# Optimization experiments

Hardware: AMD Instinct MI355X
Metric: run time of the kernel (lower is better)

## Reference

```python
import jax, jax.numpy as jnp
import numpy as np

B, M, N, D, H = 4, 8, 128, 32, 64
SMALL_V = 1e-8


def setup_inputs() -> dict:
    key = jax.random.key(0)
    ks = jax.random.split(key, 12)
    s = 0.05
    x = jax.random.normal(ks[0], (B, M, N, D), jnp.float32)
    sizes = jax.random.randint(ks[1], (B,), N // 2, N + 1)
    valid = (jnp.arange(N)[None, :] < sizes[:, None]).astype(jnp.float32)  # [B,N]
    x = x * valid[:, None, :, None]  # zero out padded items
    return {
        "x": x,
        "x_size": sizes.astype(jnp.float32),
        "W1a": jax.random.normal(ks[2], (D, 2 * D), jnp.float32) * s,
        "b1a": jax.random.normal(ks[3], (2 * D,), jnp.float32) * s,
        "W1b": jax.random.normal(ks[4], (2 * D, D), jnp.float32) * s,
        "b1b": jax.random.normal(ks[5], (D,), jnp.float32) * s,
        "W2a": jax.random.normal(ks[6], (D, 2 * D), jnp.float32) * s,
        "b2a": jax.random.normal(ks[7], (2 * D,), jnp.float32) * s,
        "W2b": jax.random.normal(ks[8], (2 * D, H), jnp.float32) * s,
        "b2b": jax.random.normal(ks[9], (H,), jnp.float32) * s,
        "w3": jax.random.normal(ks[10], (H,), jnp.float32) * s,
        "b3": jax.random.normal(ks[11], (1,), jnp.float32) * s,
    }


def _item_mask(x):
    # 1.0 where the item's feature row has any nonzero entry, else 0.0. [...,N,1]
    return jnp.any(x != 0, axis=-1, keepdims=True).astype(x.dtype)


def _set_norm(x, x_size):
    # layer_normalization with is_set_norm=True: normalize over (N*D) per set,
    # dividing by the true valid size x_size*D and masking padded items.
    b, m, n, d = x.shape
    mask = jnp.broadcast_to(_item_mask(x), x.shape).reshape(b, m, n * d)
    xr = x.reshape(b, m, n * d)
    denom = x_size[:, None] * d  # [B,1] -> broadcasts over nSet
    mean = jnp.sum(xr, axis=-1) / denom  # [B,M]
    diff = xr - mean[..., None]
    std = jnp.sqrt(jnp.sum(diff * diff * mask, axis=-1) / denom)  # [B,M]
    out = diff / (std[..., None] + SMALL_V) * mask
    return out.reshape(b, m, n, d)


def reference(x, x_size, W1a, b1a, W1b, b1b, W2a, b2a, W2b, b2b, w3, b3):
    mask = _item_mask(x)  # [B,M,N,1]
    x_orig = x
    xn = _set_norm(x, x_size) * mask  # [B,M,N,D]
    # MLP1 (rank-4 -> masked by its own input's item mask)
    m1 = _item_mask(xn)
    x1 = (jnp.matmul(jax.nn.gelu(jnp.matmul(xn, W1a) + b1a), W1b) + b1b) * m1
    # pairwise differences: x_diff[b,m,i,j,:] = x1[b,m,i,:] - xn[b,m,j,:]
    x_diff = x1[:, :, :, None, :] - xn[:, :, None, :, :]  # [B,M,N,N,D]
    # MLP2 (rank-5 -> no mask, is_SoftMax=0)
    e = jnp.matmul(jax.nn.gelu(jnp.matmul(x_diff, W2a) + b2a), W2b) + b2b  # [B,M,N,N,H]
    # aggregation: out[b,m,j,h,d] = sum_i e[b,m,i,j,h] * x1[b,m,i,d]
    agg = jnp.einsum('bmijh,bmid->bmjhd', e, x1)
    # MLP3_linear: Dense(1) over H, then squeeze
    out = jnp.einsum('bmjhd,h->bmjd', agg, w3) + b3[0]
    out = (out + x_orig) * mask
    return out
```

## Files before the change

### kernel.cpp

```cpp
#include <hip/hip_runtime.h>

#define BMC 32
#define NNC 128
#define DDC 32
#define KKC 64
constexpr int ND = NNC * DDC;
constexpr int NK = NNC * KKC;
constexpr int NS = NNC * NNC;
#define SMALLV 1e-8f

__device__ __forceinline__ float gelu_f(float v) {
    float v2 = v * v;
    float p  = fmaf(0.1029432f, v2, 2.3022082f);
    float e  = __builtin_amdgcn_exp2f(v * p);
    float r  = __builtin_amdgcn_rcpf(e + 1.0f);
    return fmaf(-v, r, v);
}

__global__ __launch_bounds__(256) void mlp_kernel(
    const float* __restrict__ x, const float* __restrict__ x_size,
    const float* __restrict__ W1a, const float* __restrict__ b1a,
    const float* __restrict__ W1b, const float* __restrict__ b1b,
    const float* __restrict__ W2a, const float* __restrict__ b2a,
    const float* __restrict__ W2b, const float* __restrict__ b2b,
    const float* __restrict__ w3,
    float* __restrict__ x1g, float* __restrict__ A1g, float* __restrict__ A2r,
    float* __restrict__ v2g, float* __restrict__ c3g)
{
    __shared__ float sW1a[DDC * KKC];
    __shared__ float sW1b[KKC * DDC];
    __shared__ float sW2a[DDC * KKC];
    __shared__ float sXn[8 * DDC];
    __shared__ float sH[8 * KKC];
    __shared__ float sX1[8 * DDC];
    __shared__ float sB1a[KKC], sB2a[KKC], sB1b[DDC];
    __shared__ float sAny[NNC];
    __shared__ float sRed[4];

    const int t  = threadIdx.x;
    const int bm = blockIdx.x >> 4;
    const int nt = blockIdx.x & 15;
    const int n0 = nt * 8;
    const int w  = t >> 6;

    {
        const float4* a4 = (const float4*)W1a;
        const float4* b4 = (const float4*)W1b;
        const float4* c4 = (const float4*)W2a;
        float4* sa = (float4*)sW1a; float4* sb = (float4*)sW1b; float4* sc = (float4*)sW2a;
        sa[t] = a4[t]; sa[t + 256] = a4[t + 256];
        sb[t] = b4[t]; sb[t + 256] = b4[t + 256];
        sc[t] = c4[t]; sc[t + 256] = c4[t + 256];
    }
    if (t < KKC) { sB1a[t] = b1a[t]; sB2a[t] = b2a[t]; }
    if (t < DDC) { sB1b[t] = b1b[t]; }
    if (t < NNC) sAny[t] = 0.f;
    __syncthreads();

    const float4* xs4 = (const float4*)(x + (size_t)bm * ND);
    float4 v4[4];
    float lsum = 0.f;
    #pragma unroll
    for (int s = 0; s < 4; ++s) {
        int f = t + s * 256;
        float4 q = xs4[f];
        v4[s] = q;
        lsum += q.x + q.y + q.z + q.w;
        if (q.x != 0.f || q.y != 0.f || q.z != 0.f || q.w != 0.f) sAny[f >> 3] = 1.f;
    }
    #pragma unroll
    for (int off = 32; off; off >>= 1) lsum += __shfl_xor(lsum, off);
    if ((t & 63) == 0) sRed[w] = lsum;
    __syncthreads();
    const float xsz   = x_size[bm >> 3];
    const float denom = xsz * (float)DDC;
    const float mean  = (sRed[0] + sRed[1] + sRed[2] + sRed[3]) / denom;

    float lsq = 0.f;
    #pragma unroll
    for (int s = 0; s < 4; ++s) {
        int f = t + s * 256;
        float mk = sAny[f >> 3];
        float dx = v4[s].x - mean, dy = v4[s].y - mean;
        float dz = v4[s].z - mean, dw = v4[s].w - mean;
        lsq += mk * (dx * dx + dy * dy + dz * dz + dw * dw);
    }
    #pragma unroll
    for (int off = 32; off; off >>= 1) lsq += __shfl_xor(lsq, off);
    __syncthreads();
    if ((t & 63) == 0) sRed[w] = lsq;
    __syncthreads();
    const float sq  = sRed[0] + sRed[1] + sRed[2] + sRed[3];
    const float inv = 1.f / (sqrtf(sq / denom) + SMALLV);

    {
        float xv = x[(size_t)bm * ND + n0 * DDC + t];
        sXn[t] = (xv - mean) * inv * sAny[n0 + (t >> 5)];
    }
    __syncthreads();

    const int k = t & 63;

    #pragma unroll
    for (int r = 0; r < 2; ++r) {
        int n = w + r * 4;
        const float* xr = &sXn[n * DDC];
        float acc = sB1a[k];
        #pragma unroll
        for (int d = 0; d < DDC; ++d) acc = fmaf(xr[d], sW1a[d * KKC + k], acc);
        sH[n * KKC + k] = gelu_f(acc);
    }
    __syncthreads();

    {
        const int d2 = t & 31;
        const int n  = t >> 5;
        const float* hr = &sH[n * KKC];
        float acc = sB1b[d2];
        #pragma unroll
        for (int q = 0; q < KKC; ++q) acc = fmaf(hr[q], sW1b[q * DDC + d2], acc);
        float val = acc * sAny[n0 + n];
        sX1[n * DDC + d2] = val;
        x1g[(size_t)bm * ND + (n0 + n) * DDC + d2] = val;
    }
    __syncthreads();

    #pragma unroll
    for (int r = 0; r < 2; ++r) {
        int n = w + r * 4;
        const float* x1r = &sX1[n * DDC];
        const float* xnr = &sXn[n * DDC];
        float a1 = sB2a[k], a2 = 0.f;
        #pragma unroll
        for (int d = 0; d < DDC; ++d) {
            a1 = fmaf(x1r[d], sW2a[d * KKC + k], a1);
            a2 = fmaf(xnr[d], sW2a[d * KKC + k], a2);
        }
        A1g[(size_t)bm * NK + (n0 + n) * KKC + k] = a1;
        A2r[(size_t)bm * NK + (n0 + n) * KKC + k] = a2;
    }

    if (blockIdx.x == 0) {
        int kk = t >> 2, hq = t & 3;
        float p = 0.f;
        #pragma unroll
        for (int h = 0; h < 16; ++h)
            p = fmaf(W2b[kk * KKC + hq * 16 + h], w3[hq * 16 + h], p);
        __syncthreads();
        sH[t] = p;
        __syncthreads();
        if (hq == 0) v2g[kk] = sH[t] + sH[t + 1] + sH[t + 2] + sH[t + 3];
        if (t < 64) {
            float q = b2b[t] * w3[t];
            #pragma unroll
            for (int off = 32; off; off >>= 1) q += __shfl_xor(q, off);
            if (t == 0) c3g[0] = q;
        }
    }
}

__global__ __launch_bounds__(256, 4) void score_kernel(
    const float* __restrict__ x_size,
    const float* __restrict__ A1g, const float* __restrict__ A2r,
    const float* __restrict__ v2g, const float* __restrict__ c3g,
    float* __restrict__ Sg)
{
    __shared__ float sA1[8 * KKC];
    __shared__ float sV2[KKC];

    const int t  = threadIdx.x;
    const int bm = blockIdx.x >> 5;
    const int jg = (blockIdx.x >> 4) & 1;
    const int ig = blockIdx.x & 15;

    const int iN = (int)(x_size[bm >> 3] + 0.5f);
    if (ig * 8 >= iN || jg * 64 >= iN) return;

    const int wv   = t >> 6;
    const int lane = t & 63;

    ((float2*)sA1)[t] = ((const float2*)(A1g + (size_t)bm * NK + ig * 8 * KKC))[t];
    if (t < KKC) sV2[t] = v2g[t];
    const float c3 = c3g[0];

    const float4* a2p = (const float4*)(A2r + (size_t)bm * NK + (jg * 64 + lane) * KKC);
    float4 a2q[16];
    #pragma unroll
    for (int q = 0; q < 16; ++q) a2q[q] = a2p[q];
    __syncthreads();

    const float4* a1f0 = (const float4*)&sA1[(wv * 2 + 0) * KKC];
    const float4* a1f1 = (const float4*)&sA1[(wv * 2 + 1) * KKC];
    const float4* v2f  = (const float4*)sV2;

    float S0 = c3, S1 = c3;
    #pragma unroll
    for (int q = 0; q < 16; ++q) {
        float4 a0 = a1f0[q];
        float4 a1 = a1f1[q];
        float4 vv = v2f[q];
        float4 b  = a2q[q];
        S0 = fmaf(gelu_f(a0.x - b.x), vv.x, S0);
        S1 = fmaf(gelu_f(a1.x - b.x), vv.x, S1);
        S0 = fmaf(gelu_f(a0.y - b.y), vv.y, S0);
        S1 = fmaf(gelu_f(a1.y - b.y), vv.y, S1);
        S0 = fmaf(gelu_f(a0.z - b.z), vv.z, S0);
        S1 = fmaf(gelu_f(a1.z - b.z), vv.z, S1);
        S0 = fmaf(gelu_f(a0.w - b.w), vv.w, S0);
        S1 = fmaf(gelu_f(a1.w - b.w), vv.w, S1);
    }
    const int i0 = ig * 8 + wv * 2;
    const int jc = jg * 64 + lane;
    Sg[(size_t)bm * NS + (i0 + 0) * NNC + jc] = S0;
    Sg[(size_t)bm * NS + (i0 + 1) * NNC + jc] = S1;
}

__global__ __launch_bounds__(256) void agg_kernel(
    const float* __restrict__ x, const float* __restrict__ x_size,
    const float* __restrict__ b3,
    const float* __restrict__ Sg, const float* __restrict__ x1g,
    float* __restrict__ out)
{
    const int gid = blockIdx.x * 256 + threadIdx.x;
    const int bm  = gid >> 12;
    const int d   = gid & 31;
    const int j   = (gid >> 5) & 127;
    const int iN  = (int)(x_size[bm >> 3] + 0.5f);
    if (j >= iN) { out[gid] = 0.f; return; }

    const float* Sp = Sg + (size_t)bm * NS + j;
    const float* xp = x1g + (size_t)bm * ND + d;
    float a0 = 0.f, a1 = 0.f, a2 = 0.f, a3 = 0.f;
    int i = 0;
    for (; i + 4 <= iN; i += 4) {
        a0 = fmaf(Sp[(i + 0) * NNC], xp[(i + 0) * DDC], a0);
        a1 = fmaf(Sp[(i + 1) * NNC], xp[(i + 1) * DDC], a1);
        a2 = fmaf(Sp[(i + 2) * NNC], xp[(i + 2) * DDC], a2);
        a3 = fmaf(Sp[(i + 3) * NNC], xp[(i + 3) * DDC], a3);
    }
    for (; i < iN; ++i) a0 = fmaf(Sp[i * NNC], xp[i * DDC], a0);
    out[gid] = (a0 + a1) + (a2 + a3) + b3[0] + x[gid];
}

extern "C" void kernel_launch(void* const* d_in, const int* in_sizes, int n_in,
                              void* d_out, int out_size, void* d_ws, size_t ws_size,
                              hipStream_t stream) {
    const float* x      = (const float*)d_in[0];
    const float* x_size = (const float*)d_in[1];
    const float* W1a    = (const float*)d_in[2];
    const float* b1a    = (const float*)d_in[3];
    const float* W1b    = (const float*)d_in[4];
    const float* b1b    = (const float*)d_in[5];
    const float* W2a    = (const float*)d_in[6];
    const float* b2a    = (const float*)d_in[7];
    const float* W2b    = (const float*)d_in[8];
    const float* b2b    = (const float*)d_in[9];
    const float* w3     = (const float*)d_in[10];
    const float* b3     = (const float*)d_in[11];
    float* out = (float*)d_out;

    float* ws  = (float*)d_ws;
    float* x1g = ws;
    float* A1g = x1g + (size_t)BMC * ND;
    float* A2r = A1g + (size_t)BMC * NK;
    float* v2g = A2r + (size_t)BMC * NK;
    float* c3g = v2g + KKC;
    float* Sg  = c3g + 64;

    mlp_kernel<<<BMC * 16, 256, 0, stream>>>(x, x_size,
        W1a, b1a, W1b, b1b, W2a, b2a, W2b, b2b, w3,
        x1g, A1g, A2r, v2g, c3g);
    score_kernel<<<BMC * 32, 256, 0, stream>>>(x_size, A1g, A2r, v2g, c3g, Sg);
    agg_kernel<<<512, 256, 0, stream>>>(x, x_size, b3, Sg, x1g, out);
}
```

Baseline: 113.1 us.

## Fuse score computation with partial aggregation, reduce i-group partials in final kernel

The score kernel now processes 16 i-rows per block (4 per wave) and immediately multiplies the scores by the matching x1 rows held in shared memory. Each block writes a 64x32 partial sum instead of a full NxN score matrix. The final kernel then adds up at most 8 partials per output rather than walking up to 128 strided score/x1 loads. This removes the NxN score round-trip through global memory and the strided aggregation reads, at the cost of more register pressure, an extra shared-memory phase and half as many blocks.

```diff
diff --git a/kernel.cpp b/kernel.cpp
--- a/kernel.cpp
+++ b/kernel.cpp
@@ -6,7 +6,6 @@
 #define KKC 64
 constexpr int ND = NNC * DDC;
 constexpr int NK = NNC * KKC;
-constexpr int NS = NNC * NNC;
 #define SMALLV 1e-8f
 
 __device__ __forceinline__ float gelu_f(float v) {
@@ -159,27 +158,30 @@
     }
 }
 
-__global__ __launch_bounds__(256, 4) void score_kernel(
+__global__ __launch_bounds__(256, 4) void pair_kernel(
     const float* __restrict__ x_size,
     const float* __restrict__ A1g, const float* __restrict__ A2r,
-    const float* __restrict__ v2g, const float* __restrict__ c3g,
-    float* __restrict__ Sg)
+    const float* __restrict__ x1g, const float* __restrict__ v2g,
+    const float* __restrict__ c3g, float* __restrict__ partial)
 {
-    __shared__ float sA1[8 * KKC];
+    __shared__ float sA1[16 * KKC];
+    __shared__ float sX1[16 * DDC];
+    __shared__ float sS[16 * 64];
     __shared__ float sV2[KKC];
 
     const int t  = threadIdx.x;
-    const int bm = blockIdx.x >> 5;
-    const int jg = (blockIdx.x >> 4) & 1;
-    const int ig = blockIdx.x & 15;
+    const int bm = blockIdx.x >> 4;
+    const int jg = (blockIdx.x >> 3) & 1;
+    const int ig = blockIdx.x & 7;
 
     const int iN = (int)(x_size[bm >> 3] + 0.5f);
-    if (ig * 8 >= iN || jg * 64 >= iN) return;
+    if (ig * 16 >= iN || jg * 64 >= iN) return;
 
     const int wv   = t >> 6;
     const int lane = t & 63;
 
-    ((float2*)sA1)[t] = ((const float2*)(A1g + (size_t)bm * NK + ig * 8 * KKC))[t];
+    ((float4*)sA1)[t] = ((const float4*)(A1g + (size_t)bm * NK + ig * 16 * KKC))[t];
+    ((float2*)sX1)[t] = ((const float2*)(x1g + (size_t)bm * ND + ig * 16 * DDC))[t];
     if (t < KKC) sV2[t] = v2g[t];
     const float c3 = c3g[0];
 
@@ -189,57 +191,90 @@
     for (int q = 0; q < 16; ++q) a2q[q] = a2p[q];
     __syncthreads();
 
-    const float4* a1f0 = (const float4*)&sA1[(wv * 2 + 0) * KKC];
-    const float4* a1f1 = (const float4*)&sA1[(wv * 2 + 1) * KKC];
-    const float4* v2f  = (const float4*)sV2;
-
-    float S0 = c3, S1 = c3;
-    #pragma unroll
-    for (int q = 0; q < 16; ++q) {
-        float4 a0 = a1f0[q];
-        float4 a1 = a1f1[q];
-        float4 vv = v2f[q];
-        float4 b  = a2q[q];
-        S0 = fmaf(gelu_f(a0.x - b.x), vv.x, S0);
-        S1 = fmaf(gelu_f(a1.x - b.x), vv.x, S1);
-        S0 = fmaf(gelu_f(a0.y - b.y), vv.y, S0);
-        S1 = fmaf(gelu_f(a1.y - b.y), vv.y, S1);
-        S0 = fmaf(gelu_f(a0.z - b.z), vv.z, S0);
-        S1 = fmaf(gelu_f(a1.z - b.z), vv.z, S1);
-        S0 = fmaf(gelu_f(a0.w - b.w), vv.w, S0);
-        S1 = fmaf(gelu_f(a1.w - b.w), vv.w, S1);
-    }
-    const int i0 = ig * 8 + wv * 2;
-    const int jc = jg * 64 + lane;
-    Sg[(size_t)bm * NS + (i0 + 0) * NNC + jc] = S0;
-    Sg[(size_t)bm * NS + (i0 + 1) * NNC + jc] = S1;
-}
-
-__global__ __launch_bounds__(256) void agg_kernel(
+    {
+        const float4* a1f0 = (const float4*)&sA1[(wv * 4 + 0) * KKC];
+        const float4* a1f1 = (const float4*)&sA1[(wv * 4 + 1) * KKC];
+        const float4* a1f2 = (const float4*)&sA1[(wv * 4 + 2) * KKC];
+        const float4* a1f3 = (const float4*)&sA1[(wv * 4 + 3) * KKC];
+        const float4* v2f  = (const float4*)sV2;
+        float S0 = c3, S1 = c3, S2 = c3, S3 = c3;
+        #pragma unroll
+        for (int q = 0; q < 16; ++q) {
+            float4 vv = v2f[q];
+            float4 a0 = a1f0[q];
+            float4 a1 = a1f1[q];
+            float4 a2 = a1f2[q];
+            float4 a3 = a1f3[q];
+            float4 b  = a2q[q];
+            S0 = fmaf(gelu_f(a0.x - b.x), vv.x, S0);
+            S1 = fmaf(gelu_f(a1.x - b.x), vv.x, S1);
+            S2 = fmaf(gelu_f(a2.x - b.x), vv.x, S2);
+            S3 = fmaf(gelu_f(a3.x - b.x), vv.x, S3);
+            S0 = fmaf(gelu_f(a0.y - b.y), vv.y, S0);
+            S1 = fmaf(gelu_f(a1.y - b.y), vv.y, S1);
+            S2 = fmaf(gelu_f(a2.y - b.y), vv.y, S2);
+            S3 = fmaf(gelu_f(a3.y - b.y), vv.y, S3);
+            S0 = fmaf(gelu_f(a0.z - b.z), vv.z, S0);
+            S1 = fmaf(gelu_f(a1.z - b.z), vv.z, S1);
+            S2 = fmaf(gelu_f(a2.z - b.z), vv.z, S2);
+            S3 = fmaf(gelu_f(a3.z - b.z), vv.z, S3);
+            S0 = fmaf(gelu_f(a0.w - b.w), vv.w, S0);
+            S1 = fmaf(gelu_f(a1.w - b.w), vv.w, S1);
+            S2 = fmaf(gelu_f(a2.w - b.w), vv.w, S2);
+            S3 = fmaf(gelu_f(a3.w - b.w), vv.w, S3);
+        }
+        sS[(wv * 4 + 0) * 64 + lane] = S0;
+        sS[(wv * 4 + 1) * 64 + lane] = S1;
+        sS[(wv * 4 + 2) * 64 + lane] = S2;
+        sS[(wv * 4 + 3) * 64 + lane] = S3;
+    }
+    __syncthreads();
+
+    {
+        const int j  = t >> 2;
+        const int dq = t & 3;
+        float acc[8];
+        #pragma unroll
+        for (int d = 0; d < 8; ++d) acc[d] = 0.f;
+        #pragma unroll
+        for (int i = 0; i < 16; ++i) {
+            float Sv = sS[i * 64 + j];
+            const float4* xf = (const float4*)&sX1[i * DDC + dq * 8];
+            float4 xa = xf[0], xb = xf[1];
+            acc[0] = fmaf(Sv, xa.x, acc[0]);
+            acc[1] = fmaf(Sv, xa.y, acc[1]);
+            acc[2] = fmaf(Sv, xa.z, acc[2]);
+            acc[3] = fmaf(Sv, xa.w, acc[3]);
+            acc[4] = fmaf(Sv, xb.x, acc[4]);
+            acc[5] = fmaf(Sv, xb.y, acc[5]);
+            acc[6] = fmaf(Sv, xb.z, acc[6]);
+            acc[7] = fmaf(Sv, xb.w, acc[7]);
+        }
+        float* pb = partial + (size_t)blockIdx.x * 2048 + t * 8;
+        ((float4*)pb)[0] = make_float4(acc[0], acc[1], acc[2], acc[3]);
+        ((float4*)pb)[1] = make_float4(acc[4], acc[5], acc[6], acc[7]);
+    }
+}
+
+__global__ __launch_bounds__(256) void final_kernel(
     const float* __restrict__ x, const float* __restrict__ x_size,
     const float* __restrict__ b3,
-    const float* __restrict__ Sg, const float* __restrict__ x1g,
-    float* __restrict__ out)
+    const float* __restrict__ partial, float* __restrict__ out)
 {
     const int gid = blockIdx.x * 256 + threadIdx.x;
     const int bm  = gid >> 12;
+    const int j   = (gid >> 5) & 127;
     const int d   = gid & 31;
-    const int j   = (gid >> 5) & 127;
     const int iN  = (int)(x_size[bm >> 3] + 0.5f);
     if (j >= iN) { out[gid] = 0.f; return; }
 
-    const float* Sp = Sg + (size_t)bm * NS + j;
-    const float* xp = x1g + (size_t)bm * ND + d;
-    float a0 = 0.f, a1 = 0.f, a2 = 0.f, a3 = 0.f;
-    int i = 0;
-    for (; i + 4 <= iN; i += 4) {
-        a0 = fmaf(Sp[(i + 0) * NNC], xp[(i + 0) * DDC], a0);
-        a1 = fmaf(Sp[(i + 1) * NNC], xp[(i + 1) * DDC], a1);
-        a2 = fmaf(Sp[(i + 2) * NNC], xp[(i + 2) * DDC], a2);
-        a3 = fmaf(Sp[(i + 3) * NNC], xp[(i + 3) * DDC], a3);
-    }
-    for (; i < iN; ++i) a0 = fmaf(Sp[i * NNC], xp[i * DDC], a0);
-    out[gid] = (a0 + a1) + (a2 + a3) + b3[0] + x[gid];
+    const int nig = (iN + 15) >> 4;
+    const int jgp = j >> 6;
+    const int jl  = j & 63;
+    const size_t pb = ((size_t)(bm * 2 + jgp) * 8) * 2048 + jl * 32 + d;
+    float sum = 0.f;
+    for (int ig = 0; ig < nig; ++ig) sum += partial[pb + (size_t)ig * 2048];
+    out[gid] = sum + b3[0] + x[gid];
 }
 
 extern "C" void kernel_launch(void* const* d_in, const int* in_sizes, int n_in,
@@ -259,17 +294,17 @@
     const float* b3     = (const float*)d_in[11];
     float* out = (float*)d_out;
 
-    float* ws  = (float*)d_ws;
-    float* x1g = ws;
-    float* A1g = x1g + (size_t)BMC * ND;
-    float* A2r = A1g + (size_t)BMC * NK;
-    float* v2g = A2r + (size_t)BMC * NK;
-    float* c3g = v2g + KKC;
-    float* Sg  = c3g + 64;
+    float* ws      = (float*)d_ws;
+    float* x1g     = ws;
+    float* A1g     = x1g + (size_t)BMC * ND;
+    float* A2r     = A1g + (size_t)BMC * NK;
+    float* v2g     = A2r + (size_t)BMC * NK;
+    float* c3g     = v2g + KKC;
+    float* partial = c3g + 64;
 
     mlp_kernel<<<BMC * 16, 256, 0, stream>>>(x, x_size,
         W1a, b1a, W1b, b1b, W2a, b2a, W2b, b2b, w3,
         x1g, A1g, A2r, v2g, c3g);
-    score_kernel<<<BMC * 32, 256, 0, stream>>>(x_size, A1g, A2r, v2g, c3g, Sg);
-    agg_kernel<<<512, 256, 0, stream>>>(x, x_size, b3, Sg, x1g, out);
-}
+    pair_kernel<<<BMC * 16, 256, 0, stream>>>(x_size, A1g, A2r, x1g, v2g, c3g, partial);
+    final_kernel<<<512, 256, 0, stream>>>(x, x_size, b3, partial, out);
+}
```

After: 104.7 us. 7.4% less time.
